# Kernel optimization log

Hardware: AMD Instinct MI355X
Metric: run time of the kernel (lower is better)

## Reference

```python
import jax, jax.numpy as jnp
import numpy as np

B, N = 2048, 4096

def setup_inputs() -> dict:
    key = jax.random.key(0)
    k1, k2, k3, k4, k5 = jax.random.split(key, 5)
    scale = 1.0 / np.sqrt(N)  # match nn.Linear init scale
    return {
        "t": jnp.zeros((1,), dtype=jnp.float32),
        "y": jax.random.uniform(k1, (B, N), dtype=jnp.float32),
        "W1": jax.random.normal(k2, (N, N), dtype=jnp.float32) * scale,
        "b1": jax.random.normal(k3, (N,), dtype=jnp.float32) * scale,
        "W2": jax.random.normal(k4, (N, N), dtype=jnp.float32) * scale,
        "b2": jax.random.normal(k5, (N,), dtype=jnp.float32) * scale,
    }

def reference(t, y, W1, b1, W2, b2):
    # out = fcc2(fcc1(y)) : two Linear layers (y @ W^T + b)
    h = y @ W1.T + b1            # [B, N]
    out = h @ W2.T + b2          # [B, N]
    # f = ones(N,1) @ y @ out^T  ==  dot(y, out) broadcast over N;
    # dydt = y * (out - dot(y, out))   (replicator equation)
    dot = jnp.sum(y * out, axis=-1, keepdims=True)  # [B, 1]
    return y * (out - dot)       # [B, N]
```

## Files before the change

kernel.cpp:

```cpp
#include <hip/hip_runtime.h>
#include <hip/hip_bf16.h>
#include <stdint.h>

typedef _Float16 f16;
typedef _Float16 f16x4 __attribute__((ext_vector_type(4)));
typedef _Float16 f16x8 __attribute__((ext_vector_type(8)));
typedef float f32x4 __attribute__((ext_vector_type(4)));

#define ASYNC_COPY16(gsrc, ldst)                                                   \
    __builtin_amdgcn_global_load_lds(                                              \
        (__attribute__((address_space(1))) void*)(gsrc),                           \
        (__attribute__((address_space(3))) void*)(ldst), 16, 0, 0)

__global__ __launch_bounds__(256) void cvt_f32_to_f16(const float* __restrict__ in,
                                                      f16* __restrict__ out, int n4) {
    int i = blockIdx.x * 256 + threadIdx.x;
    if (i >= n4) return;
    float4 v = ((const float4*)in)[i];
    f16x4 o;
    o.x = (f16)v.x; o.y = (f16)v.y; o.z = (f16)v.z; o.w = (f16)v.w;
    ((f16x4*)out)[i] = o;
}

__global__ __launch_bounds__(256) void cvt3_f32_to_f16(const float* __restrict__ y,
                                                       const float* __restrict__ W1,
                                                       const float* __restrict__ W2,
                                                       f16* __restrict__ yb,
                                                       f16* __restrict__ w1b,
                                                       f16* __restrict__ w2b,
                                                       int nY4, int nW4) {
    int i = blockIdx.x * 256 + threadIdx.x;
    const float* src;
    f16* dst;
    int off;
    if (i < nY4) {
        src = y; dst = yb; off = i;
    } else if (i < nY4 + nW4) {
        src = W1; dst = w1b; off = i - nY4;
    } else {
        src = W2; dst = w2b; off = i - nY4 - nW4;
        if (off >= nW4) return;
    }
    float4 v = ((const float4*)src)[off];
    f16x4 o;
    o.x = (f16)v.x; o.y = (f16)v.y; o.z = (f16)v.z; o.w = (f16)v.w;
    ((f16x4*)dst)[off] = o;
}

template <int STORE_F16>
__global__ __launch_bounds__(256) void gemm_bt(const f16* __restrict__ A,
                                               const f16* __restrict__ Bm,
                                               const float* __restrict__ bias,
                                               void* __restrict__ Cout,
                                               int M, int N, int K) {
    constexpr int BM = 128, BN = 128, BK = 64;
    __shared__ __align__(16) f16 sA[2][BM * BK];
    __shared__ __align__(16) f16 sB[2][BN * BK];

    const int tid   = threadIdx.x;
    const int lane  = tid & 63;
    const int wave  = tid >> 6;
    const int waveM = wave >> 1;
    const int waveN = wave & 1;

    const int bm = blockIdx.y * BM;
    const int bn = blockIdx.x * BN;

    const f16* Aptr = A + (size_t)bm * K;
    const f16* Bptr = Bm + (size_t)bn * K;

    const int srow_lo = tid >> 3;
    const int sseg    = tid & 7;

    f32x4 acc[4][4] = {};

    const int quad = lane >> 4;
    const int l16  = lane & 15;

    const int iters = K / BK;

    {
#pragma unroll
        for (int j = 0; j < 4; j++) {
            const int row = j * 32 + srow_lo;
            const int seg = sseg ^ (row & 7);
            ASYNC_COPY16(Aptr + (size_t)row * K + 0 + seg * 8, &sA[0][j * 2048 + tid * 8]);
        }
#pragma unroll
        for (int j = 0; j < 4; j++) {
            const int row = j * 32 + srow_lo;
            const int seg = sseg ^ (row & 7);
            ASYNC_COPY16(Bptr + (size_t)row * K + 0 + seg * 8, &sB[0][j * 2048 + tid * 8]);
        }
    }

    int cur = 0;
    for (int it = 0; it < iters; ++it) {
        __syncthreads();

        if (it + 1 < iters) {
            const int k0 = (it + 1) * BK;
#pragma unroll
            for (int j = 0; j < 4; j++) {
                const int row = j * 32 + srow_lo;
                const int seg = sseg ^ (row & 7);
                ASYNC_COPY16(Aptr + (size_t)row * K + k0 + seg * 8,
                             &sA[cur ^ 1][j * 2048 + tid * 8]);
            }
#pragma unroll
            for (int j = 0; j < 4; j++) {
                const int row = j * 32 + srow_lo;
                const int seg = sseg ^ (row & 7);
                ASYNC_COPY16(Bptr + (size_t)row * K + k0 + seg * 8,
                             &sB[cur ^ 1][j * 2048 + tid * 8]);
            }
        }

#pragma unroll
        for (int h = 0; h < 2; h++) {
            f16x8 af[4], bf[4];
#pragma unroll
            for (int mi = 0; mi < 4; mi++) {
                const int row = waveM * 64 + mi * 16 + l16;
                const int seg = (h * 4 + quad) ^ (row & 7);
                af[mi] = *(const f16x8*)&sA[cur][row * BK + seg * 8];
            }
#pragma unroll
            for (int ni = 0; ni < 4; ni++) {
                const int row = waveN * 64 + ni * 16 + l16;
                const int seg = (h * 4 + quad) ^ (row & 7);
                bf[ni] = *(const f16x8*)&sB[cur][row * BK + seg * 8];
            }
#pragma unroll
            for (int mi = 0; mi < 4; mi++)
#pragma unroll
                for (int ni = 0; ni < 4; ni++)
                    acc[mi][ni] = __builtin_amdgcn_mfma_f32_16x16x32_f16(af[mi], bf[ni],
                                                                         acc[mi][ni], 0, 0, 0);
        }
        cur ^= 1;
    }

#pragma unroll
    for (int ni = 0; ni < 4; ni++) {
        const int col = bn + waveN * 64 + ni * 16 + l16;
        const float bv = bias[col];
#pragma unroll
        for (int mi = 0; mi < 4; mi++) {
            const int row0 = bm + waveM * 64 + mi * 16 + quad * 4;
#pragma unroll
            for (int r = 0; r < 4; r++) {
                float v = acc[mi][ni][r] + bv;
                if (STORE_F16)
                    ((f16*)Cout)[(size_t)(row0 + r) * N + col] = (f16)v;
                else
                    ((float*)Cout)[(size_t)(row0 + r) * N + col] = v;
            }
        }
    }
}

__global__ __launch_bounds__(256) void replicator(const float* __restrict__ y,
                                                  float* __restrict__ out, int N) {
    const int row = blockIdx.x;
    const float4* y4 = (const float4*)(y + (size_t)row * N);
    float4* o4 = (float4*)(out + (size_t)row * N);
    const int n4 = N / 4;

    float p = 0.f;
    for (int i = threadIdx.x; i < n4; i += 256) {
        float4 a = y4[i], b = o4[i];
        p += a.x * b.x + a.y * b.y + a.z * b.z + a.w * b.w;
    }
#pragma unroll
    for (int off = 32; off > 0; off >>= 1) p += __shfl_down(p, off, 64);

    __shared__ float sred[4];
    if ((threadIdx.x & 63) == 0) sred[threadIdx.x >> 6] = p;
    __syncthreads();
    const float dot = sred[0] + sred[1] + sred[2] + sred[3];

    for (int i = threadIdx.x; i < n4; i += 256) {
        float4 a = y4[i], b = o4[i];
        float4 r;
        r.x = a.x * (b.x - dot);
        r.y = a.y * (b.y - dot);
        r.z = a.z * (b.z - dot);
        r.w = a.w * (b.w - dot);
        o4[i] = r;
    }
}

extern "C" void kernel_launch(void* const* d_in, const int* in_sizes, int n_in,
                              void* d_out, int out_size, void* d_ws, size_t ws_size,
                              hipStream_t stream) {
    const float* y  = (const float*)d_in[1];
    const float* W1 = (const float*)d_in[2];
    const float* b1 = (const float*)d_in[3];
    const float* W2 = (const float*)d_in[4];
    const float* b2 = (const float*)d_in[5];

    const int N = in_sizes[3];
    const int B = in_sizes[1] / N;
    float* out = (float*)d_out;

    const size_t szY = (size_t)B * N;
    const size_t szW = (size_t)N * N;

    const int yn4 = (int)(szY / 4);
    const int wn4 = (int)(szW / 4);

    dim3 g1(N / 128, B / 128);

    const size_t need_big = (szY + 2 * szW + szY) * sizeof(f16);

    if (ws_size >= need_big) {
        f16* yb  = (f16*)d_ws;
        f16* w1b = yb + szY;
        f16* w2b = w1b + szW;
        f16* hb  = w2b + szW;

        const int tot4 = yn4 + 2 * wn4;
        cvt3_f32_to_f16<<<(tot4 + 255) / 256, 256, 0, stream>>>(y, W1, W2, yb, w1b, w2b,
                                                                yn4, wn4);
        gemm_bt<1><<<g1, 256, 0, stream>>>(yb, w1b, b1, hb, B, N, N);
        gemm_bt<0><<<g1, 256, 0, stream>>>(hb, w2b, b2, out, B, N, N);
    } else {
        f16* yb = (f16*)d_ws;
        f16* wb = yb + szY;
        f16* hb = wb + szW;

        cvt_f32_to_f16<<<yn4 / 256, 256, 0, stream>>>(y, yb, yn4);
        cvt_f32_to_f16<<<wn4 / 256, 256, 0, stream>>>(W1, wb, wn4);
        gemm_bt<1><<<g1, 256, 0, stream>>>(yb, wb, b1, hb, B, N, N);
        cvt_f32_to_f16<<<wn4 / 256, 256, 0, stream>>>(W2, wb, wn4);
        gemm_bt<0><<<g1, 256, 0, stream>>>(hb, wb, b2, out, B, N, N);
    }

    replicator<<<B, 256, 0, stream>>>(y, out, N);
}
```

Baseline: 349.0 us.

## Fuse row dot product into second GEMM epilogue and remap tiles per XCD

The second GEMM's epilogue now multiplies each output element by the matching y value, reduces within 16 lanes, and atomically adds the partial into a per-row dot buffer. The replicator kernel therefore no longer makes a separate read pass to compute the dot. Block indices are also remapped so each XCD works on a contiguous range of column tiles, which is meant to improve L2 reuse of the B operand. In exchange this adds a memset, float atomics (nondeterministic summation order), and an extra read of fp32 y inside the GEMM epilogue.

```diff
diff --git a/kernel.cpp b/kernel.cpp
--- a/kernel.cpp
+++ b/kernel.cpp
@@ -47,11 +47,13 @@
     ((f16x4*)dst)[off] = o;
 }
 
-template <int STORE_F16>
+template <int STORE_F16, int FUSE_DOT>
 __global__ __launch_bounds__(256) void gemm_bt(const f16* __restrict__ A,
                                                const f16* __restrict__ Bm,
                                                const float* __restrict__ bias,
                                                void* __restrict__ Cout,
+                                               const float* __restrict__ Yf,
+                                               float* __restrict__ dotv,
                                                int M, int N, int K) {
     constexpr int BM = 128, BN = 128, BK = 64;
     __shared__ __align__(16) f16 sA[2][BM * BK];
@@ -63,8 +65,24 @@
     const int waveM = wave >> 1;
     const int waveN = wave & 1;
 
-    const int bm = blockIdx.y * BM;
-    const int bn = blockIdx.x * BN;
+    int bxt, byt;
+    {
+        const int p = blockIdx.y * gridDim.x + blockIdx.x;
+        if ((gridDim.x & 7) == 0) {
+            const int xcd  = p & 7;
+            const int slot = p >> 3;
+            const int cpx  = gridDim.x >> 3;
+            const int c    = slot / gridDim.y;
+            const int r    = slot - c * gridDim.y;
+            bxt = xcd * cpx + c;
+            byt = r;
+        } else {
+            bxt = blockIdx.x;
+            byt = blockIdx.y;
+        }
+    }
+    const int bm = byt * BM;
+    const int bn = bxt * BN;
 
     const f16* Aptr = A + (size_t)bm * K;
     const f16* Bptr = Bm + (size_t)bn * K;
@@ -79,19 +97,17 @@
 
     const int iters = K / BK;
 
-    {
-#pragma unroll
-        for (int j = 0; j < 4; j++) {
-            const int row = j * 32 + srow_lo;
-            const int seg = sseg ^ (row & 7);
-            ASYNC_COPY16(Aptr + (size_t)row * K + 0 + seg * 8, &sA[0][j * 2048 + tid * 8]);
-        }
-#pragma unroll
-        for (int j = 0; j < 4; j++) {
-            const int row = j * 32 + srow_lo;
-            const int seg = sseg ^ (row & 7);
-            ASYNC_COPY16(Bptr + (size_t)row * K + 0 + seg * 8, &sB[0][j * 2048 + tid * 8]);
-        }
+#pragma unroll
+    for (int j = 0; j < 4; j++) {
+        const int row = j * 32 + srow_lo;
+        const int seg = sseg ^ (row & 7);
+        ASYNC_COPY16(Aptr + (size_t)row * K + seg * 8, &sA[0][j * 2048 + tid * 8]);
+    }
+#pragma unroll
+    for (int j = 0; j < 4; j++) {
+        const int row = j * 32 + srow_lo;
+        const int seg = sseg ^ (row & 7);
+        ASYNC_COPY16(Bptr + (size_t)row * K + seg * 8, &sB[0][j * 2048 + tid * 8]);
     }
 
     int cur = 0;
@@ -142,44 +158,40 @@
     }
 
 #pragma unroll
-    for (int ni = 0; ni < 4; ni++) {
-        const int col = bn + waveN * 64 + ni * 16 + l16;
-        const float bv = bias[col];
-#pragma unroll
-        for (int mi = 0; mi < 4; mi++) {
-            const int row0 = bm + waveM * 64 + mi * 16 + quad * 4;
-#pragma unroll
-            for (int r = 0; r < 4; r++) {
-                float v = acc[mi][ni][r] + bv;
+    for (int mi = 0; mi < 4; mi++) {
+#pragma unroll
+        for (int r = 0; r < 4; r++) {
+            const int row = bm + waveM * 64 + mi * 16 + quad * 4 + r;
+            float rowsum = 0.f;
+#pragma unroll
+            for (int ni = 0; ni < 4; ni++) {
+                const int col = bn + waveN * 64 + ni * 16 + l16;
+                float v = acc[mi][ni][r] + bias[col];
                 if (STORE_F16)
-                    ((f16*)Cout)[(size_t)(row0 + r) * N + col] = (f16)v;
+                    ((f16*)Cout)[(size_t)row * N + col] = (f16)v;
                 else
-                    ((float*)Cout)[(size_t)(row0 + r) * N + col] = v;
-            }
-        }
-    }
-}
-
-__global__ __launch_bounds__(256) void replicator(const float* __restrict__ y,
-                                                  float* __restrict__ out, int N) {
+                    ((float*)Cout)[(size_t)row * N + col] = v;
+                if (FUSE_DOT) rowsum += v * Yf[(size_t)row * N + col];
+            }
+            if (FUSE_DOT) {
+#pragma unroll
+                for (int off = 8; off > 0; off >>= 1)
+                    rowsum += __shfl_xor(rowsum, off, 64);
+                if (l16 == 0) atomicAdd(&dotv[row], rowsum);
+            }
+        }
+    }
+}
+
+__global__ __launch_bounds__(256) void finish_replicator(const float* __restrict__ y,
+                                                         float* __restrict__ out,
+                                                         const float* __restrict__ dotv,
+                                                         int N) {
     const int row = blockIdx.x;
+    const float dot = dotv[row];
     const float4* y4 = (const float4*)(y + (size_t)row * N);
     float4* o4 = (float4*)(out + (size_t)row * N);
     const int n4 = N / 4;
-
-    float p = 0.f;
-    for (int i = threadIdx.x; i < n4; i += 256) {
-        float4 a = y4[i], b = o4[i];
-        p += a.x * b.x + a.y * b.y + a.z * b.z + a.w * b.w;
-    }
-#pragma unroll
-    for (int off = 32; off > 0; off >>= 1) p += __shfl_down(p, off, 64);
-
-    __shared__ float sred[4];
-    if ((threadIdx.x & 63) == 0) sred[threadIdx.x >> 6] = p;
-    __syncthreads();
-    const float dot = sred[0] + sred[1] + sred[2] + sred[3];
-
     for (int i = threadIdx.x; i < n4; i += 256) {
         float4 a = y4[i], b = o4[i];
         float4 r;
@@ -212,30 +224,34 @@
 
     dim3 g1(N / 128, B / 128);
 
-    const size_t need_big = (szY + 2 * szW + szY) * sizeof(f16);
+    const size_t need_big = (szY + 2 * szW + szY) * sizeof(f16) + (size_t)B * 4;
 
     if (ws_size >= need_big) {
         f16* yb  = (f16*)d_ws;
         f16* w1b = yb + szY;
         f16* w2b = w1b + szW;
         f16* hb  = w2b + szW;
+        float* dotv = (float*)(hb + szY);
 
         const int tot4 = yn4 + 2 * wn4;
         cvt3_f32_to_f16<<<(tot4 + 255) / 256, 256, 0, stream>>>(y, W1, W2, yb, w1b, w2b,
                                                                 yn4, wn4);
-        gemm_bt<1><<<g1, 256, 0, stream>>>(yb, w1b, b1, hb, B, N, N);
-        gemm_bt<0><<<g1, 256, 0, stream>>>(hb, w2b, b2, out, B, N, N);
+        hipMemsetAsync(dotv, 0, (size_t)B * 4, stream);
+        gemm_bt<1, 0><<<g1, 256, 0, stream>>>(yb, w1b, b1, hb, nullptr, nullptr, B, N, N);
+        gemm_bt<0, 1><<<g1, 256, 0, stream>>>(hb, w2b, b2, out, y, dotv, B, N, N);
+        finish_replicator<<<B, 256, 0, stream>>>(y, out, dotv, N);
     } else {
         f16* yb = (f16*)d_ws;
         f16* wb = yb + szY;
         f16* hb = wb + szW;
+        float* dotv = (float*)(hb + szY);
 
         cvt_f32_to_f16<<<yn4 / 256, 256, 0, stream>>>(y, yb, yn4);
         cvt_f32_to_f16<<<wn4 / 256, 256, 0, stream>>>(W1, wb, wn4);
-        gemm_bt<1><<<g1, 256, 0, stream>>>(yb, wb, b1, hb, B, N, N);
+        hipMemsetAsync(dotv, 0, (size_t)B * 4, stream);
+        gemm_bt<1, 0><<<g1, 256, 0, stream>>>(yb, wb, b1, hb, nullptr, nullptr, B, N, N);
         cvt_f32_to_f16<<<wn4 / 256, 256, 0, stream>>>(W2, wb, wn4);
-        gemm_bt<0><<<g1, 256, 0, stream>>>(hb, wb, b2, out, B, N, N);
-    }
-
-    replicator<<<B, 256, 0, stream>>>(y, out, N);
-}
+        gemm_bt<0, 1><<<g1, 256, 0, stream>>>(hb, wb, b2, out, y, dotv, B, N, N);
+        finish_replicator<<<B, 256, 0, stream>>>(y, out, dotv, N);
+    }
+}
```

Result: no change. 355.5 us (+1.9%).
